# Kernel optimization log

Hardware: AMD Instinct MI355X
Metric: run time of the kernel (lower is better)

The kernel has to match this reference:

```python
import jax, jax.numpy as jnp
import numpy as np

DIM = 2048
N_HEADS = 16
QK_NOPE = 128
QK_ROPE = 64
V_DIM = 128
QK_DIM = QK_NOPE + QK_ROPE  # 192
B, S = 2, 2048


def setup_inputs() -> dict:
    key = jax.random.key(0)
    ks = jax.random.split(key, 6)
    x = jax.random.normal(ks[0], (B, S, DIM), dtype=jnp.float32)
    # rotary angles: theta[j] = 10000^{-2j/d}, angle[p, j] = p * theta[j]
    inv_freq = 1.0 / (10000.0 ** (np.arange(0, QK_ROPE, 2, dtype=np.float32) / QK_ROPE))
    freqs = jnp.asarray(np.arange(S, dtype=np.float32)[:, None] * inv_freq[None, :])  # [S, QK_ROPE//2]
    # additive causal mask
    mask = jnp.where(jnp.tril(jnp.ones((S, S), dtype=bool)), 0.0, -1e9).astype(jnp.float32)
    sc = 1.0 / np.sqrt(DIM)
    wq = jax.random.normal(ks[1], (DIM, N_HEADS * QK_DIM), dtype=jnp.float32) * sc
    wk = jax.random.normal(ks[2], (DIM, N_HEADS * QK_DIM), dtype=jnp.float32) * sc
    wv = jax.random.normal(ks[3], (DIM, N_HEADS * V_DIM), dtype=jnp.float32) * sc
    wo = jax.random.normal(ks[4], (N_HEADS * V_DIM, DIM), dtype=jnp.float32) * (1.0 / np.sqrt(N_HEADS * V_DIM))
    return {"x": x, "start_pos": 0, "freqs": freqs, "mask": mask,
            "wq": wq, "wk": wk, "wv": wv, "wo": wo}


def _apply_rope(t, freqs):
    # t: [B, S, H, D_rope]; freqs: [S, D_rope//2] angles
    b, s, h, d = t.shape
    tr = t.reshape(b, s, h, d // 2, 2)
    cos = jnp.cos(freqs)[None, :, None, :]
    sin = jnp.sin(freqs)[None, :, None, :]
    out = jnp.stack([tr[..., 0] * cos - tr[..., 1] * sin,
                     tr[..., 0] * sin + tr[..., 1] * cos], axis=-1)
    return out.reshape(b, s, h, d)


def reference(x, start_pos, freqs, mask, wq, wk, wv, wo):
    b, s, _ = x.shape
    xq = x @ wq  # [B,S,H*QK_DIM]
    xk = x @ wk
    xv = (x @ wv).reshape(b, s, N_HEADS, V_DIM)
    qnope, qrope = jnp.split(xq, [N_HEADS * QK_NOPE], axis=-1)
    knope, krope = jnp.split(xk, [N_HEADS * QK_NOPE], axis=-1)
    qnope = qnope.reshape(b, s, N_HEADS, QK_NOPE)
    knope = knope.reshape(b, s, N_HEADS, QK_NOPE)
    qrope = _apply_rope(qrope.reshape(b, s, N_HEADS, QK_ROPE), freqs)
    krope = _apply_rope(krope.reshape(b, s, N_HEADS, QK_ROPE), freqs)
    q = jnp.concatenate([qnope, qrope], axis=-1)  # [B,S,H,QK_DIM]
    k = jnp.concatenate([knope, krope], axis=-1)
    scale = 1.0 / jnp.sqrt(jnp.asarray(QK_DIM, dtype=q.dtype))
    scores = jnp.einsum('bqhd,bkhd->bhqk', q, k) * scale
    scores = scores + mask[None, None, :, :]
    attn = jax.nn.softmax(scores.astype(jnp.float32), axis=-1).astype(scores.dtype)
    out = jnp.einsum('bhqk,bkhd->bqhd', attn, xv)  # [B,S,H,V_DIM]
    out = out.reshape(b, s, N_HEADS * V_DIM)
    return out @ wo
```

## Files before the change

### kernel.cpp

```cpp
#include <hip/hip_runtime.h>
#include <hip/hip_bf16.h>

typedef __attribute__((ext_vector_type(4))) float f32x4;
typedef __attribute__((ext_vector_type(8))) short s16x8;
typedef unsigned int u32;
typedef unsigned short u16;

#define GLDS16(gp, lp) __builtin_amdgcn_global_load_lds(                         \
    (const __attribute__((address_space(1))) u32*)(gp),                          \
    (__attribute__((address_space(3))) u32*)(lp), 16, 0, 0)
#define VMCNT4 asm volatile("s_waitcnt vmcnt(4)" ::: "memory")
#define VMCNT0 asm volatile("s_waitcnt vmcnt(0)" ::: "memory")
#define LGKM8  asm volatile("s_waitcnt lgkmcnt(8)" ::: "memory")
#define LGKM0  asm volatile("s_waitcnt lgkmcnt(0)" ::: "memory")
#define SBAR   __builtin_amdgcn_sched_barrier(0)

__device__ __forceinline__ u16 f2bf(float f) {
    u32 u = __builtin_bit_cast(u32, f);
    u32 r = (u + 0x7FFFu + ((u >> 16) & 1u)) >> 16;
    return (u16)r;
}
__device__ __forceinline__ float bf2f(u16 h) {
    u32 u = ((u32)h) << 16;
    return __builtin_bit_cast(float, u);
}

__global__ __launch_bounds__(256) void prep(const float4* __restrict__ x,
                                            ushort4* __restrict__ xb4,
                                            const float* __restrict__ wq,
                                            const float* __restrict__ wk,
                                            const float* __restrict__ wv,
                                            const float* __restrict__ wo,
                                            u16* __restrict__ WT,
                                            u16* __restrict__ woT) {
    __shared__ float tile[32][132];
    int bid = blockIdx.x;
    if (bid < 8192) {
        int i = bid * 256 + threadIdx.x;
        float4 v = x[i];
        ushort4 o;
        o.x = f2bf(v.x); o.y = f2bf(v.y); o.z = f2bf(v.z); o.w = f2bf(v.w);
        xb4[i] = o;
        return;
    }
    bid -= 8192;
    const float* src;
    u16* dst;
    int N, bx, by;
    if (bid < 1536)      { src = wq; dst = WT;                         N = 3072; bx = bid % 24; by = bid / 24; }
    else if (bid < 3072) { bid -= 1536; src = wk; dst = WT + (size_t)3072 * 2048; N = 3072; bx = bid % 24; by = bid / 24; }
    else if (bid < 4096) { bid -= 3072; src = wv; dst = WT + (size_t)6144 * 2048; N = 2048; bx = bid % 16; by = bid / 16; }
    else                 { bid -= 4096; src = wo; dst = woT;           N = 2048; bx = bid % 16; by = bid / 16; }
    int n0 = bx * 128, k0 = by * 32;
    int nf = threadIdx.x & 31, kr = threadIdx.x >> 5;
#pragma unroll
    for (int i = 0; i < 4; ++i) {
        int row = kr + i * 8;
        float4 v = *(const float4*)&src[(size_t)(k0 + row) * N + n0 + 4 * nf];
        tile[row][4 * nf + 0] = v.x;
        tile[row][4 * nf + 1] = v.y;
        tile[row][4 * nf + 2] = v.z;
        tile[row][4 * nf + 3] = v.w;
    }
    __syncthreads();
    int kk = threadIdx.x & 31, nr0 = threadIdx.x >> 5;
#pragma unroll
    for (int i = 0; i < 16; ++i) {
        int n = nr0 + i * 8;
        dst[(size_t)(n0 + n) * 2048 + k0 + kk] = f2bf(tile[kk][n]);
    }
}

__global__ __launch_bounds__(512, 2) void gemm_qkv(const u16* __restrict__ A,
                                                   const u16* __restrict__ W,
                                                   u16* __restrict__ Qh,
                                                   u16* __restrict__ Kh,
                                                   u16* __restrict__ Vn) {
    __shared__ __align__(16) u16 S[2][2][2][128 * 64];
    const int tid = threadIdx.x, lane = tid & 63, wid = tid >> 6;
    const int l15 = lane & 15, l4 = lane >> 4;
    const int id = blockIdx.x;
    const int nt = ((id & 7) << 2) + ((id >> 3) & 3);
    const int mt = id >> 5;
    const int bm0 = mt << 8, bn0 = nt << 8;
    const int wr = wid >> 2, wc = wid & 3;
    f32x4 acc[8][4] = {};

    auto stageH = [&](int mat, int tt, int h) {
        const int kc = tt << 6, p = tt & 1;
        const u16* G = mat ? W : A;
        const int rbase = (mat ? bn0 : bm0) + (h << 7);
        u16* Ld = S[mat][p][h];
#pragma unroll
        for (int j = 0; j < 2; ++j) {
            int c = j * 512 + tid;
            int row = c >> 3, ch = c & 7;
            int cs = ch ^ (row & 7);
            GLDS16(G + (size_t)(rbase + row) * 2048 + kc + cs * 8,
                   (char*)Ld + (j * 512 + wid * 64) * 16);
        }
    };

    s16x8 af[2][2], bfr[4][2];

#define RDA(P, I)                                                              \
    _Pragma("unroll") for (int mm = 0; mm < 2; ++mm)                           \
    _Pragma("unroll") for (int kk = 0; kk < 2; ++kk) {                         \
        int r7 = ((I) * 2 + mm) * 16 + l15;                                    \
        int byt = r7 * 128 + (((kk * 4 + l4) ^ (r7 & 7)) << 4);                \
        af[mm][kk] = *(const s16x8*)((const char*)S[0][P][wr] + byt);          \
    }
#define RDB(P)                                                                 \
    _Pragma("unroll") for (int n = 0; n < 4; ++n)                              \
    _Pragma("unroll") for (int kk = 0; kk < 2; ++kk) {                         \
        int r7 = (wc & 1) * 64 + n * 16 + l15;                                 \
        int byt = r7 * 128 + (((kk * 4 + l4) ^ (r7 & 7)) << 4);                \
        bfr[n][kk] = *(const s16x8*)((const char*)S[1][P][wc >> 1] + byt);     \
    }
#define MF(I)                                                                  \
    __builtin_amdgcn_s_setprio(1);                                             \
    _Pragma("unroll") for (int mm = 0; mm < 2; ++mm)                           \
    _Pragma("unroll") for (int n = 0; n < 4; ++n)                              \
    _Pragma("unroll") for (int kk = 0; kk < 2; ++kk)                           \
        acc[(I) * 2 + mm][n] = __builtin_amdgcn_mfma_f32_16x16x32_bf16(        \
            af[mm][kk], bfr[n][kk], acc[(I) * 2 + mm][n], 0, 0, 0);            \
    __builtin_amdgcn_s_setprio(0);

    stageH(0, 0, 0); stageH(0, 0, 1); stageH(1, 0, 0); stageH(1, 0, 1);
    stageH(0, 1, 0); stageH(0, 1, 1);
    VMCNT4;
    __builtin_amdgcn_s_barrier();
    SBAR;

    for (int t = 0; t < 32; ++t) {
        const int p = t & 1;
        RDB(p); RDA(p, 0);
        if (t == 0) stageH(1, 1, 0);
        else if (t < 31) stageH(0, t + 1, 0);
        LGKM8; SBAR;
        __builtin_amdgcn_s_barrier();
        LGKM0; SBAR;
        MF(0); SBAR;
        __builtin_amdgcn_s_barrier();
        RDA(p, 1);
        if (t == 0) stageH(1, 1, 1);
        else if (t < 31) stageH(0, t + 1, 1);
        __builtin_amdgcn_s_barrier();
        LGKM0; SBAR;
        MF(1); SBAR;
        __builtin_amdgcn_s_barrier();
        RDA(p, 2);
        if (t < 30) stageH(1, t + 2, 0);
        __builtin_amdgcn_s_barrier();
        LGKM0; SBAR;
        MF(2); SBAR;
        __builtin_amdgcn_s_barrier();
        RDA(p, 3);
        if (t < 30) stageH(1, t + 2, 1);
        __builtin_amdgcn_s_barrier();
        LGKM0; SBAR;
        MF(3); SBAR;
        if (t < 31) {
            if (t < 30) { VMCNT4; } else { VMCNT0; }
            SBAR;
        }
        __builtin_amdgcn_s_barrier();
    }
#undef RDA
#undef RDB
#undef MF

#pragma unroll
    for (int m = 0; m < 8; ++m)
#pragma unroll
        for (int n = 0; n < 4; ++n)
#pragma unroll
            for (int r = 0; r < 4; ++r) {
                int row = bm0 + wr * 128 + m * 16 + l4 * 4 + r;
                int c = bn0 + wc * 64 + n * 16 + l15;
                float v = acc[m][n][r];
                if (bn0 >= 6144) {
                    Vn[(size_t)row * 2048 + (c - 6144)] = f2bf(v);
                } else {
                    u16* dst = (bn0 >= 3072) ? Kh : Qh;
                    int cc = (bn0 >= 3072) ? c - 3072 : c;
                    int b = row >> 11, s = row & 2047;
                    int h, d;
                    if (cc < 2048) { h = cc >> 7; d = cc & 127; }
                    else { int mm = cc - 2048; h = mm >> 6; d = 128 + (mm & 63); }
                    dst[(((size_t)b * 16 + h) * 2048 + s) * 192 + d] = f2bf(v);
                }
            }
}

__global__ __launch_bounds__(256) void gemm_bt_f32(const u16* __restrict__ A,
                                                   const u16* __restrict__ Bt,
                                                   float* __restrict__ C,
                                                   int M, int N, int K) {
    __shared__ __align__(16) u16 As[128 * 64];
    __shared__ __align__(16) u16 Bs[128 * 64];
    const int tid = threadIdx.x, lane = tid & 63, wid = tid >> 6;
    const int l15 = lane & 15, l4 = lane >> 4;
    const int bm0 = blockIdx.y << 7, bn0 = blockIdx.x << 7;
    const int wr = wid >> 1, wc = wid & 1;
    f32x4 acc[4][4] = {};
    const int nk = K >> 6;
    for (int t = 0; t < nk; ++t) {
        const int k0 = t << 6;
#pragma unroll
        for (int i = 0; i < 4; ++i) {
            int c = i * 256 + tid;
            int row = c >> 3, c8 = c & 7;
            GLDS16(A + (size_t)(bm0 + row) * K + k0 + c8 * 8,
                   (char*)As + (i * 256 + wid * 64) * 16);
        }
#pragma unroll
        for (int i = 0; i < 4; ++i) {
            int c = i * 256 + tid;
            int row = c >> 3, c8 = c & 7;
            GLDS16(Bt + (size_t)(bn0 + row) * K + k0 + c8 * 8,
                   (char*)Bs + (i * 256 + wid * 64) * 16);
        }
        __syncthreads();
#pragma unroll
        for (int kk = 0; kk < 64; kk += 32) {
            s16x8 af[4], bfr[4];
#pragma unroll
            for (int m = 0; m < 4; ++m)
                af[m] = *(const s16x8*)(As + (wr * 64 + m * 16 + l15) * 64 + kk + l4 * 8);
#pragma unroll
            for (int n = 0; n < 4; ++n)
                bfr[n] = *(const s16x8*)(Bs + (wc * 64 + n * 16 + l15) * 64 + kk + l4 * 8);
#pragma unroll
            for (int m = 0; m < 4; ++m)
#pragma unroll
                for (int n = 0; n < 4; ++n)
                    acc[m][n] = __builtin_amdgcn_mfma_f32_16x16x32_bf16(af[m], bfr[n],
                                                                        acc[m][n], 0, 0, 0);
        }
        __syncthreads();
    }
#pragma unroll
    for (int m = 0; m < 4; ++m)
#pragma unroll
        for (int n = 0; n < 4; ++n)
#pragma unroll
            for (int r = 0; r < 4; ++r) {
                int row = bm0 + wr * 64 + m * 16 + l4 * 4 + r;
                int col = bn0 + wc * 64 + n * 16 + l15;
                C[(size_t)row * N + col] = acc[m][n][r];
            }
}

__global__ __launch_bounds__(256) void rope_qk(u16* __restrict__ Qh,
                                               u16* __restrict__ Kh,
                                               const float* __restrict__ freqs) {
    int idx = blockIdx.x * 256 + threadIdx.x;
    int j = idx & 31, s = (idx >> 5) & 2047, bh = idx >> 16;
    float ang = freqs[s * 32 + j];
    float c = cosf(ang), sn = sinf(ang);
    size_t off = ((size_t)bh * 2048 + s) * 192 + 128;
    u32* pq = (u32*)(Qh + off) + j;
    u32* pk = (u32*)(Kh + off) + j;
    u32 vq = *pq, vk = *pk;
    float q0 = bf2f((u16)(vq & 0xffff)), q1 = bf2f((u16)(vq >> 16));
    float k0 = bf2f((u16)(vk & 0xffff)), k1 = bf2f((u16)(vk >> 16));
    *pq = (u32)f2bf(q0 * c - q1 * sn) | ((u32)f2bf(q0 * sn + q1 * c) << 16);
    *pk = (u32)f2bf(k0 * c - k1 * sn) | ((u32)f2bf(k0 * sn + k1 * c) << 16);
}

__global__ __launch_bounds__(256) void vtrans(const u16* __restrict__ Vn,
                                              u16* __restrict__ Vt) {
    __shared__ u16 tile[32][33];
    int s0 = blockIdx.x * 32, d0 = blockIdx.y * 32, bh = blockIdx.z;
    int b = bh >> 4, h = bh & 15;
    int tx = threadIdx.x & 31, ty = threadIdx.x >> 5;
#pragma unroll
    for (int i = 0; i < 4; ++i) {
        int s = ty + i * 8;
        tile[s][tx] = Vn[((size_t)b * 2048 + s0 + s) * 2048 + h * 128 + d0 + tx];
    }
    __syncthreads();
#pragma unroll
    for (int i = 0; i < 4; ++i) {
        int d = ty + i * 8;
        Vt[((size_t)bh * 128 + d0 + d) * 2048 + s0 + tx] = tile[tx][d];
    }
}

__global__ __launch_bounds__(256) void attn_fwd3(const u16* __restrict__ Qh,
                                                 const u16* __restrict__ Kh,
                                                 const u16* __restrict__ Vt,
                                                 u16* __restrict__ AO) {
    __shared__ __align__(16) u16 Ks[64 * 192];
    __shared__ __align__(16) u16 Vs[128 * 64];
    __shared__ __align__(16) u16 Ps[4][32 * 64];
    const int tid = threadIdx.x, lane = tid & 63, wid = tid >> 6;
    const int l15 = lane & 15, l4 = lane >> 4;
    const int id = blockIdx.x;
    const int bh = id & 31;
    const int qt = 15 - (id >> 5);
    const int q0 = qt << 7;
    const u16* Qb = Qh + ((size_t)bh * 2048 + q0 + wid * 32) * 192;
    const u16* Kb = Kh + (size_t)bh * 2048 * 192;
    const u16* Vb = Vt + (size_t)bh * 128 * 2048;

    s16x8 aq[2][6];
#pragma unroll
    for (int qg = 0; qg < 2; ++qg)
#pragma unroll
        for (int dk = 0; dk < 6; ++dk)
            aq[qg][dk] = *(const s16x8*)(Qb + (size_t)(qg * 16 + l15) * 192 + dk * 32 + l4 * 8);

    f32x4 acc[2][8] = {};
    float mrow[2][4], lpart[2][4];
#pragma unroll
    for (int qg = 0; qg < 2; ++qg)
#pragma unroll
        for (int r = 0; r < 4; ++r) { mrow[qg][r] = -1e30f; lpart[qg][r] = 0.f; }
    const float scale = 0.07216878364870322f;

    const int ntile = (qt + 1) << 1;
    for (int t = 0; t < ntile; ++t) {
        const int k0 = t << 6;
#pragma unroll
        for (int i = 0; i < 6; ++i) {
            int c = i * 256 + tid;
            int row = (u32)c / 24u, cc = c - row * 24;
            int cs = (cc & 24) | ((cc ^ row) & 7);
            GLDS16(Kb + (size_t)(k0 + row) * 192 + cs * 8,
                   (char*)Ks + (i * 256 + wid * 64) * 16);
        }
#pragma unroll
        for (int i = 0; i < 4; ++i) {
            int c = i * 256 + tid;
            int d = c >> 3, cc = c & 7;
            int cs = cc ^ (d & 7);
            GLDS16(Vb + (size_t)d * 2048 + k0 + cs * 8,
                   (char*)Vs + (i * 256 + wid * 64) * 16);
        }
        __syncthreads();

        if (q0 + wid * 32 + 31 >= k0) {
            f32x4 sc[2][4];
#pragma unroll
            for (int qg = 0; qg < 2; ++qg)
#pragma unroll
                for (int kg = 0; kg < 4; ++kg) sc[qg][kg] = f32x4{0.f, 0.f, 0.f, 0.f};
            __builtin_amdgcn_s_setprio(1);
#pragma unroll
            for (int dk = 0; dk < 6; ++dk) {
                s16x8 bk[4];
#pragma unroll
                for (int kg = 0; kg < 4; ++kg) {
                    int row = kg * 16 + l15;
                    int byt = (row * 384 + dk * 64 + l4 * 16) ^ ((row & 7) << 4);
                    bk[kg] = *(const s16x8*)((const char*)Ks + byt);
                }
#pragma unroll
                for (int qg = 0; qg < 2; ++qg)
#pragma unroll
                    for (int kg = 0; kg < 4; ++kg)
                        sc[qg][kg] = __builtin_amdgcn_mfma_f32_16x16x32_bf16(
                            aq[qg][dk], bk[kg], sc[qg][kg], 0, 0, 0);
            }
            __builtin_amdgcn_s_setprio(0);

            u16* Pw = Ps[wid];
#pragma unroll
            for (int qg = 0; qg < 2; ++qg) {
                const int qrow = q0 + wid * 32 + qg * 16 + l4 * 4;
                const bool domask = (k0 + 63 > qrow);
                float p[4][4], tm[4];
#pragma unroll
                for (int r = 0; r < 4; ++r) tm[r] = -1e30f;
#pragma unroll
                for (int kg = 0; kg < 4; ++kg)
#pragma unroll
                    for (int r = 0; r < 4; ++r) {
                        float v = sc[qg][kg][r] * scale;
                        if (domask && (k0 + kg * 16 + l15 > qrow + r)) v = -1e30f;
                        p[kg][r] = v;
                        tm[r] = fmaxf(tm[r], v);
                    }
#pragma unroll
                for (int off = 1; off < 16; off <<= 1)
#pragma unroll
                    for (int r = 0; r < 4; ++r)
                        tm[r] = fmaxf(tm[r], __shfl_xor(tm[r], off, 64));
                float mn[4];
                bool resc = false;
#pragma unroll
                for (int r = 0; r < 4; ++r) {
                    mn[r] = (tm[r] <= mrow[qg][r] + 8.f) ? mrow[qg][r] : tm[r];
                    resc |= (mn[r] > mrow[qg][r]);
                }
                if (__any(resc)) {
#pragma unroll
                    for (int r = 0; r < 4; ++r) {
                        float scl = __expf(mrow[qg][r] - mn[r]);
                        mrow[qg][r] = mn[r];
                        lpart[qg][r] *= scl;
#pragma unroll
                        for (int db = 0; db < 8; ++db) acc[qg][db][r] *= scl;
                    }
                }
#pragma unroll
                for (int kg = 0; kg < 4; ++kg)
#pragma unroll
                    for (int r = 0; r < 4; ++r) {
                        p[kg][r] = __expf(p[kg][r] - mrow[qg][r]);
                        lpart[qg][r] += p[kg][r];
                    }
#pragma unroll
                for (int kg = 0; kg < 4; ++kg)
#pragma unroll
                    for (int r = 0; r < 4; ++r) {
                        int row = qg * 16 + l4 * 4 + r;
                        int byt = ((row * 64 + kg * 16 + l15) * 2) ^ ((row & 7) << 4);
                        *(u16*)((char*)Pw + byt) = f2bf(p[kg][r]);
                    }
            }

            __builtin_amdgcn_s_setprio(1);
#pragma unroll
            for (int kk = 0; kk < 2; ++kk) {
                s16x8 ap[2];
#pragma unroll
                for (int qg = 0; qg < 2; ++qg) {
                    int row = qg * 16 + l15;
                    int byt = ((row * 64 + kk * 32 + l4 * 8) * 2) ^ ((row & 7) << 4);
                    ap[qg] = *(const s16x8*)((const char*)Pw + byt);
                }
#pragma unroll
                for (int db = 0; db < 8; ++db) {
                    int row = db * 16 + l15;
                    int byt = (row * 128 + kk * 64 + l4 * 16) ^ ((row & 7) << 4);
                    s16x8 bv = *(const s16x8*)((const char*)Vs + byt);
#pragma unroll
                    for (int qg = 0; qg < 2; ++qg)
                        acc[qg][db] = __builtin_amdgcn_mfma_f32_16x16x32_bf16(
                            ap[qg], bv, acc[qg][db], 0, 0, 0);
                }
            }
            __builtin_amdgcn_s_setprio(0);
        }
        __syncthreads();
    }

#pragma unroll
    for (int off = 1; off < 16; off <<= 1)
#pragma unroll
        for (int qg = 0; qg < 2; ++qg)
#pragma unroll
            for (int r = 0; r < 4; ++r)
                lpart[qg][r] += __shfl_xor(lpart[qg][r], off, 64);

    const int b = bh >> 4, h = bh & 15;
#pragma unroll
    for (int qg = 0; qg < 2; ++qg) {
        float inv[4];
#pragma unroll
        for (int r = 0; r < 4; ++r) inv[r] = 1.f / lpart[qg][r];
#pragma unroll
        for (int db = 0; db < 8; ++db)
#pragma unroll
            for (int r = 0; r < 4; ++r) {
                int row = q0 + wid * 32 + qg * 16 + l4 * 4 + r;
                AO[((size_t)b * 2048 + row) * 2048 + h * 128 + db * 16 + l15] =
                    f2bf(acc[qg][db][r] * inv[r]);
            }
    }
}

extern "C" void kernel_launch(void* const* d_in, const int* in_sizes, int n_in,
                              void* d_out, int out_size, void* d_ws, size_t ws_size,
                              hipStream_t stream) {
    const float* x     = (const float*)d_in[0];
    const float* freqs = (const float*)d_in[2];
    const float* wq    = (const float*)d_in[4];
    const float* wk    = (const float*)d_in[5];
    const float* wv    = (const float*)d_in[6];
    const float* wo    = (const float*)d_in[7];
    float* out = (float*)d_out;

    char* ws = (char*)d_ws;
    u16* xb   = (u16*)(ws + 0);
    u16* WT   = (u16*)(ws + 16777216);
    u16* woT  = (u16*)(ws + 50331648);
    u16* Qh   = (u16*)(ws + 58720256);
    u16* Kh   = (u16*)(ws + 83886080);
    u16* Vn   = (u16*)(ws + 109051904);
    u16* Vt   = (u16*)(ws + 125829120);
    u16* AO   = (u16*)(ws + 142606336);

    prep<<<13312, 256, 0, stream>>>((const float4*)x, (ushort4*)xb,
                                    wq, wk, wv, wo, WT, woT);
    gemm_qkv<<<dim3(512), 512, 0, stream>>>(xb, WT, Qh, Kh, Vn);
    rope_qk<<<8192, 256, 0, stream>>>(Qh, Kh, freqs);
    vtrans<<<dim3(64, 4, 32), 256, 0, stream>>>(Vn, Vt);
    attn_fwd3<<<dim3(512), 256, 0, stream>>>(Qh, Kh, Vt, AO);
    gemm_bt_f32<<<dim3(16, 32), 256, 0, stream>>>(AO, woT, out, 4096, 2048, 2048);
}
```

Measured before the change: 340.6 us.

## Rewrite output projection GEMM with 256x128 tiles, double-buffered swizzled LDS pipeline

Replaces the simple single-buffered 128x128 output-projection GEMM with an 8-wave 256x128 tile kernel. It double-buffers A/B tiles in LDS, XOR-swizzles LDS chunks to avoid bank conflicts, and interleaves async global-to-LDS loads for the next k-step with MFMA phases, using s_setprio around the compute. The aim is to hide global latency and cut the per-iteration syncthreads stalls in the final GEMM. In exchange it hardcodes M/N/K and relies on fine-grained barriers and vmcnt counting that must match the issue order exactly.

```diff
diff --git a/kernel.cpp b/kernel.cpp
--- a/kernel.cpp
+++ b/kernel.cpp
@@ -10,6 +10,7 @@
     (const __attribute__((address_space(1))) u32*)(gp),                          \
     (__attribute__((address_space(3))) u32*)(lp), 16, 0, 0)
 #define VMCNT4 asm volatile("s_waitcnt vmcnt(4)" ::: "memory")
+#define VMCNT2 asm volatile("s_waitcnt vmcnt(2)" ::: "memory")
 #define VMCNT0 asm volatile("s_waitcnt vmcnt(0)" ::: "memory")
 #define LGKM8  asm volatile("s_waitcnt lgkmcnt(8)" ::: "memory")
 #define LGKM0  asm volatile("s_waitcnt lgkmcnt(0)" ::: "memory")
@@ -193,62 +194,119 @@
             }
 }
 
-__global__ __launch_bounds__(256) void gemm_bt_f32(const u16* __restrict__ A,
+__global__ __launch_bounds__(512, 2) void gemm_bt8(const u16* __restrict__ A,
                                                    const u16* __restrict__ Bt,
-                                                   float* __restrict__ C,
-                                                   int M, int N, int K) {
-    __shared__ __align__(16) u16 As[128 * 64];
-    __shared__ __align__(16) u16 Bs[128 * 64];
+                                                   float* __restrict__ C) {
+    __shared__ __align__(16) u16 SA[2][2][128 * 64];
+    __shared__ __align__(16) u16 SB[2][2][64 * 64];
     const int tid = threadIdx.x, lane = tid & 63, wid = tid >> 6;
     const int l15 = lane & 15, l4 = lane >> 4;
-    const int bm0 = blockIdx.y << 7, bn0 = blockIdx.x << 7;
-    const int wr = wid >> 1, wc = wid & 1;
-    f32x4 acc[4][4] = {};
-    const int nk = K >> 6;
-    for (int t = 0; t < nk; ++t) {
-        const int k0 = t << 6;
-#pragma unroll
-        for (int i = 0; i < 4; ++i) {
-            int c = i * 256 + tid;
-            int row = c >> 3, c8 = c & 7;
-            GLDS16(A + (size_t)(bm0 + row) * K + k0 + c8 * 8,
-                   (char*)As + (i * 256 + wid * 64) * 16);
-        }
-#pragma unroll
-        for (int i = 0; i < 4; ++i) {
-            int c = i * 256 + tid;
-            int row = c >> 3, c8 = c & 7;
-            GLDS16(Bt + (size_t)(bn0 + row) * K + k0 + c8 * 8,
-                   (char*)Bs + (i * 256 + wid * 64) * 16);
-        }
-        __syncthreads();
-#pragma unroll
-        for (int kk = 0; kk < 64; kk += 32) {
-            s16x8 af[4], bfr[4];
-#pragma unroll
-            for (int m = 0; m < 4; ++m)
-                af[m] = *(const s16x8*)(As + (wr * 64 + m * 16 + l15) * 64 + kk + l4 * 8);
-#pragma unroll
-            for (int n = 0; n < 4; ++n)
-                bfr[n] = *(const s16x8*)(Bs + (wc * 64 + n * 16 + l15) * 64 + kk + l4 * 8);
-#pragma unroll
-            for (int m = 0; m < 4; ++m)
-#pragma unroll
-                for (int n = 0; n < 4; ++n)
-                    acc[m][n] = __builtin_amdgcn_mfma_f32_16x16x32_bf16(af[m], bfr[n],
-                                                                        acc[m][n], 0, 0, 0);
-        }
-        __syncthreads();
-    }
-#pragma unroll
-    for (int m = 0; m < 4; ++m)
-#pragma unroll
-        for (int n = 0; n < 4; ++n)
+    const int bid = blockIdx.x;
+    const int bm0 = (bid >> 4) << 8, bn0 = (bid & 15) << 7;
+    const int wr = wid >> 2, wc = wid & 3;
+    f32x4 acc[8][2] = {};
+
+    auto stageA = [&](int tt, int h) {
+        const int kc = tt << 6, p = tt & 1;
+        const int rbase = bm0 + (h << 7);
+        u16* Ld = SA[p][h];
+#pragma unroll
+        for (int j = 0; j < 2; ++j) {
+            int c = j * 512 + tid;
+            int row = c >> 3, ch = c & 7;
+            int cs = ch ^ (row & 7);
+            GLDS16(A + (size_t)(rbase + row) * 2048 + kc + cs * 8,
+                   (char*)Ld + (j * 512 + wid * 64) * 16);
+        }
+    };
+    auto stageB = [&](int tt, int h) {
+        const int kc = tt << 6, p = tt & 1;
+        const int rbase = bn0 + (h << 6);
+        u16* Ld = SB[p][h];
+        int row = tid >> 3, ch = tid & 7;
+        int cs = ch ^ (row & 7);
+        GLDS16(Bt + (size_t)(rbase + row) * 2048 + kc + cs * 8,
+               (char*)Ld + (wid * 64) * 16);
+    };
+
+    s16x8 af[2][2], bfr[2][2];
+
+#define RDA2(P, I)                                                             \
+    _Pragma("unroll") for (int mm = 0; mm < 2; ++mm)                           \
+    _Pragma("unroll") for (int kk = 0; kk < 2; ++kk) {                         \
+        int r7 = ((I) * 2 + mm) * 16 + l15;                                    \
+        int byt = r7 * 128 + (((kk * 4 + l4) ^ (r7 & 7)) << 4);                \
+        af[mm][kk] = *(const s16x8*)((const char*)SA[P][wr] + byt);            \
+    }
+#define RDB2(P)                                                                \
+    _Pragma("unroll") for (int n = 0; n < 2; ++n)                              \
+    _Pragma("unroll") for (int kk = 0; kk < 2; ++kk) {                         \
+        int r7 = (wc & 1) * 32 + n * 16 + l15;                                 \
+        int byt = r7 * 128 + (((kk * 4 + l4) ^ (r7 & 7)) << 4);                \
+        bfr[n][kk] = *(const s16x8*)((const char*)SB[P][wc >> 1] + byt);       \
+    }
+#define MF2(I)                                                                 \
+    __builtin_amdgcn_s_setprio(1);                                             \
+    _Pragma("unroll") for (int mm = 0; mm < 2; ++mm)                           \
+    _Pragma("unroll") for (int n = 0; n < 2; ++n)                              \
+    _Pragma("unroll") for (int kk = 0; kk < 2; ++kk)                           \
+        acc[(I) * 2 + mm][n] = __builtin_amdgcn_mfma_f32_16x16x32_bf16(        \
+            af[mm][kk], bfr[n][kk], acc[(I) * 2 + mm][n], 0, 0, 0);            \
+    __builtin_amdgcn_s_setprio(0);
+
+    stageA(0, 0); stageA(0, 1); stageB(0, 0); stageB(0, 1);
+    stageA(1, 0); stageA(1, 1);
+    VMCNT4;
+    __builtin_amdgcn_s_barrier();
+    SBAR;
+
+    for (int t = 0; t < 32; ++t) {
+        const int p = t & 1;
+        RDB2(p); RDA2(p, 0);
+        if (t == 0) stageB(1, 0);
+        else if (t < 31) stageA(t + 1, 0);
+        SBAR;
+        __builtin_amdgcn_s_barrier();
+        LGKM0; SBAR;
+        MF2(0); SBAR;
+        __builtin_amdgcn_s_barrier();
+        RDA2(p, 1);
+        if (t == 0) stageB(1, 1);
+        else if (t < 31) stageA(t + 1, 1);
+        __builtin_amdgcn_s_barrier();
+        LGKM0; SBAR;
+        MF2(1); SBAR;
+        __builtin_amdgcn_s_barrier();
+        RDA2(p, 2);
+        if (t < 30) stageB(t + 2, 0);
+        __builtin_amdgcn_s_barrier();
+        LGKM0; SBAR;
+        MF2(2); SBAR;
+        __builtin_amdgcn_s_barrier();
+        RDA2(p, 3);
+        if (t < 30) stageB(t + 2, 1);
+        __builtin_amdgcn_s_barrier();
+        LGKM0; SBAR;
+        MF2(3); SBAR;
+        if (t < 31) {
+            if (t < 30) { VMCNT2; } else { VMCNT0; }
+            SBAR;
+        }
+        __builtin_amdgcn_s_barrier();
+    }
+#undef RDA2
+#undef RDB2
+#undef MF2
+
+#pragma unroll
+    for (int m = 0; m < 8; ++m)
+#pragma unroll
+        for (int n = 0; n < 2; ++n)
 #pragma unroll
             for (int r = 0; r < 4; ++r) {
-                int row = bm0 + wr * 64 + m * 16 + l4 * 4 + r;
-                int col = bn0 + wc * 64 + n * 16 + l15;
-                C[(size_t)row * N + col] = acc[m][n][r];
+                int row = bm0 + wr * 128 + m * 16 + l4 * 4 + r;
+                int col = bn0 + wc * 32 + n * 16 + l15;
+                C[(size_t)row * 2048 + col] = acc[m][n][r];
             }
 }
 
@@ -500,5 +558,5 @@
     rope_qk<<<8192, 256, 0, stream>>>(Qh, Kh, freqs);
     vtrans<<<dim3(64, 4, 32), 256, 0, stream>>>(Vn, Vt);
     attn_fwd3<<<dim3(512), 256, 0, stream>>>(Qh, Kh, Vt, AO);
-    gemm_bt_f32<<<dim3(16, 32), 256, 0, stream>>>(AO, woT, out, 4096, 2048, 2048);
-}
+    gemm_bt8<<<dim3(256), 512, 0, stream>>>(AO, woT, out);
+}
```

Result: no change. 343.4 us (+0.8%).
